# Kernel tuning notes

Measured on AMD Instinct MI355X. Metric: run time of the kernel, lower is better.

The kernel has to match this reference:

```python
import jax, jax.numpy as jnp
import numpy as np

B, Z, H, T = 256, 512, 1024, 512   # batch, z_size, hidden (conductor==decoder), num_tokens
L, N = 16, 16                      # num_levels, notes_per_bar


def setup_inputs() -> dict:
    key = jax.random.key(0)
    ks = jax.random.split(key, 16)
    s = 0.05  # weight init scale
    rn = lambda k, shp, sc=1.0: sc * jax.random.normal(k, shp, dtype=jnp.float32)
    return {
        "z": rn(ks[0], (B, L * N, 1, Z)),
        "dec_h0": rn(ks[1], (L, B, H)),
        "dec_c0": rn(ks[2], (L, B, H)),
        # linear_in (computed but unused by the original forward)
        "lin_in_W": rn(ks[3], (Z, Z), s), "lin_in_b": rn(ks[4], (Z,), s),
        # conductor LSTM (input Z -> hidden H), PyTorch gate order i,f,g,o
        "cond_Wih": rn(ks[5], (4 * H, Z), s), "cond_Whh": rn(ks[6], (4 * H, H), s),
        "cond_bih": rn(ks[7], (4 * H,), s), "cond_bhh": rn(ks[8], (4 * H,), s),
        # decoder LSTM (input T+H -> hidden H)
        "dec_Wih": rn(ks[9], (4 * H, T + H), s), "dec_Whh": rn(ks[10], (4 * H, H), s),
        "dec_bih": rn(ks[11], (4 * H,), s), "dec_bhh": rn(ks[12], (4 * H,), s),
        # output projection
        "out_W": rn(ks[13], (T, H), s), "out_b": rn(ks[14], (T,), s),
    }


def _lstm_cell(x, h, c, Wih, Whh, b):
    gates = x @ Wih.T + h @ Whh.T + b            # [B, 4H]
    i, f, g, o = jnp.split(gates, 4, axis=-1)
    c = jax.nn.sigmoid(f) * c + jax.nn.sigmoid(i) * jnp.tanh(g)
    h = jax.nn.sigmoid(o) * jnp.tanh(c)
    return h, c


def reference(z, dec_h0, dec_c0, lin_in_W, lin_in_b,
              cond_Wih, cond_Whh, cond_bih, cond_bhh,
              dec_Wih, dec_Whh, dec_bih, dec_bhh, out_W, out_b):
    Bsz = z.shape[0]
    Tt = out_b.shape[0]
    Hh = cond_Whh.shape[1]

    _unused = z @ lin_in_W.T + lin_in_b  # linear_in output is discarded in the source

    cond_b = cond_bih + cond_bhh
    dec_b = dec_bih + dec_bhh

    # conductor consumes z[:, L*level, 0, :] for each level
    z_lv = jnp.transpose(z[:, jnp.arange(L) * L, 0, :], (1, 0, 2))  # [L, B, Z]

    def level_step(carry, xs):
        ch, cc = carry
        zl, dh, dc = xs
        ch, cc = _lstm_cell(zl, ch, cc, cond_Wih, cond_Whh, cond_b)
        emb = ch  # [B, H], fixed conductor embedding for this bar

        def note_step(c2, _):
            note, dh2, dc2 = c2
            inp = jnp.concatenate([emb, note], axis=-1)  # [B, H+T]
            dh2, dc2 = _lstm_cell(inp, dh2, dc2, dec_Wih, dec_Whh, dec_b)
            out = jax.nn.sigmoid(dh2 @ out_W.T + out_b)  # [B, T]
            return (out, dh2, dc2), out

        note0 = jnp.zeros((Bsz, Tt), dtype=z.dtype)
        _, outs = jax.lax.scan(note_step, (note0, dh, dc), None, length=N)  # [N, B, T]
        return (ch, cc), outs

    h0 = jnp.zeros((Bsz, Hh), dtype=z.dtype)
    _, all_outs = jax.lax.scan(level_step, (h0, h0), (z_lv, dec_h0, dec_c0))  # [L, N, B, T]
    notes = jnp.transpose(all_outs, (2, 0, 1, 3)).reshape(Bsz, L * N, Tt)
    return notes
```

## Files before the change

### kernel.cpp

```cpp
#include <hip/hip_runtime.h>

typedef __bf16 bf16;
typedef __attribute__((ext_vector_type(8))) __bf16 bf16x8;
typedef __attribute__((ext_vector_type(4))) float f32x4;

__device__ __forceinline__ void gload_lds16(const void* g, void* l) {
  __builtin_amdgcn_global_load_lds(
      (const __attribute__((address_space(1))) void*)g,
      (__attribute__((address_space(3))) void*)l, 16, 0, 0);
}

__device__ __forceinline__ float sigmoidf_(float x) { return 1.0f / (1.0f + expf(-x)); }

template<int BM, int BN, int WM, int WN, int MODE>
__global__ __launch_bounds__(WM * WN * 64)
void gemm_bt(const bf16* __restrict__ A, int lda,
             const bf16* __restrict__ Bw, int ldb,
             float* __restrict__ C, int ldc,
             int K,
             const float* __restrict__ outb, float* __restrict__ dout,
             bf16* __restrict__ anote, int nstep) {
  constexpr int BK = 64;
  constexpr int THREADS = WM * WN * 64;
  constexpr int SM = BM / WM, SN = BN / WN;
  constexpr int FM = SM / 16, FN = SN / 16;

  __shared__ __align__(16) bf16 lsA[BM * BK];
  __shared__ __align__(16) bf16 lsB[BN * BK];

  const int tid = threadIdx.x;
  const int lane = tid & 63;
  const int wave = tid >> 6;
  const int wm = wave / WN, wn = wave % WN;
  const int m0 = blockIdx.y * BM;
  const int n0 = blockIdx.x * BN;

  f32x4 acc[FM][FN] = {};

  const bf16* gA = A + (size_t)m0 * lda;
  const bf16* gB = Bw + (size_t)n0 * ldb;

  for (int k0 = 0; k0 < K; k0 += BK) {
#pragma unroll
    for (int i = 0; i < (BM * 8) / THREADS; ++i) {
      int idx = i * THREADS + tid;
      gload_lds16(gA + (size_t)(idx >> 3) * lda + k0 + (idx & 7) * 8, &lsA[idx * 8]);
    }
#pragma unroll
    for (int i = 0; i < (BN * 8) / THREADS; ++i) {
      int idx = i * THREADS + tid;
      gload_lds16(gB + (size_t)(idx >> 3) * ldb + k0 + (idx & 7) * 8, &lsB[idx * 8]);
    }
    __syncthreads();

#pragma unroll
    for (int kk = 0; kk < BK; kk += 32) {
      bf16x8 av[FM], bv[FN];
#pragma unroll
      for (int i = 0; i < FM; ++i)
        av[i] = *(const bf16x8*)&lsA[(wm * SM + i * 16 + (lane & 15)) * BK + kk + (lane >> 4) * 8];
#pragma unroll
      for (int j = 0; j < FN; ++j)
        bv[j] = *(const bf16x8*)&lsB[(wn * SN + j * 16 + (lane & 15)) * BK + kk + (lane >> 4) * 8];
#pragma unroll
      for (int i = 0; i < FM; ++i)
#pragma unroll
        for (int j = 0; j < FN; ++j)
          acc[i][j] = __builtin_amdgcn_mfma_f32_16x16x32_bf16(av[i], bv[j], acc[i][j], 0, 0, 0);
    }
    __syncthreads();
  }

#pragma unroll
  for (int i = 0; i < FM; ++i) {
#pragma unroll
    for (int j = 0; j < FN; ++j) {
      const int col = n0 + wn * SN + j * 16 + (lane & 15);
      const int rbase = m0 + wm * SM + i * 16 + ((lane >> 4) << 2);
#pragma unroll
      for (int r = 0; r < 4; ++r) {
        const int row = rbase + r;
        float v = acc[i][j][r];
        if constexpr (MODE == 0) {
          C[(size_t)row * ldc + col] = v;
        } else if constexpr (MODE == 2) {
          ((bf16*)C)[(size_t)row * ldc + col] = (bf16)v;
        } else {
          v = sigmoidf_(v + outb[col]);
          const int l = row >> 8, b = row & 255;
          dout[((size_t)(b * 256 + l * 16 + nstep)) * 512 + col] = v;
          anote[(size_t)row * 1536 + col] = (bf16)v;
        }
      }
    }
  }
}

template<int BM, int BJ, int WM, int WJ>
__global__ __launch_bounds__(WM * WJ * 64, 2)
void gemm_cell(const bf16* __restrict__ A, int lda,
               const bf16* __restrict__ Bw,
               const bf16* __restrict__ X,
               const float* __restrict__ bias,
               float* __restrict__ cst,
               bf16* __restrict__ hout, int ldh, int K) {
  constexpr int BK = 64;
  constexpr int THREADS = WM * WJ * 64;
  constexpr int BN = BJ * 64;
  constexpr int SM = BM / WM;
  constexpr int TJ = BJ / WJ;
  constexpr int FM = SM / 16;

  __shared__ __align__(16) bf16 lsA[BM * BK];
  __shared__ __align__(16) bf16 lsB[BN * BK];

  const int tid = threadIdx.x;
  const int lane = tid & 63;
  const int wave = tid >> 6;
  const int wm = wave / WJ, wj = wave % WJ;
  const int m0 = blockIdx.y * BM;
  const int qb = blockIdx.x * BJ;

  f32x4 acc[FM][TJ][4] = {};

  const bf16* gA = A + (size_t)m0 * lda;
  const bf16* gB = Bw + (size_t)(qb * 64) * K;

  for (int k0 = 0; k0 < K; k0 += BK) {
#pragma unroll
    for (int i = 0; i < (BM * 8) / THREADS; ++i) {
      int idx = i * THREADS + tid;
      gload_lds16(gA + (size_t)(idx >> 3) * lda + k0 + (idx & 7) * 8, &lsA[idx * 8]);
    }
#pragma unroll
    for (int i = 0; i < (BN * 8) / THREADS; ++i) {
      int idx = i * THREADS + tid;
      gload_lds16(gB + (size_t)(idx >> 3) * K + k0 + (idx & 7) * 8, &lsB[idx * 8]);
    }
    __syncthreads();

#pragma unroll
    for (int kk = 0; kk < BK; kk += 32) {
      bf16x8 av[FM], bv[TJ][4];
#pragma unroll
      for (int i = 0; i < FM; ++i)
        av[i] = *(const bf16x8*)&lsA[(wm * SM + i * 16 + (lane & 15)) * BK + kk + (lane >> 4) * 8];
#pragma unroll
      for (int t = 0; t < TJ; ++t)
#pragma unroll
        for (int g = 0; g < 4; ++g)
          bv[t][g] = *(const bf16x8*)
              &lsB[((wj * TJ + t) * 64 + g * 16 + (lane & 15)) * BK + kk + (lane >> 4) * 8];
#pragma unroll
      for (int i = 0; i < FM; ++i)
#pragma unroll
        for (int t = 0; t < TJ; ++t)
#pragma unroll
          for (int g = 0; g < 4; ++g)
            acc[i][t][g] =
                __builtin_amdgcn_mfma_f32_16x16x32_bf16(av[i], bv[t][g], acc[i][t][g], 0, 0, 0);
    }
    __syncthreads();
  }

#pragma unroll
  for (int i = 0; i < FM; ++i) {
#pragma unroll
    for (int t = 0; t < TJ; ++t) {
      const int q = qb + wj * TJ + t;
      const int jj = lane & 15;
      const int j = q * 16 + jj;
      const int rbase = m0 + wm * SM + i * 16 + ((lane >> 4) << 2);
      const float b0 = bias[q * 64 + jj];
      const float b1 = bias[q * 64 + 16 + jj];
      const float b2 = bias[q * 64 + 32 + jj];
      const float b3 = bias[q * 64 + 48 + jj];
#pragma unroll
      for (int r = 0; r < 4; ++r) {
        const int row = rbase + r;
        const bf16* xp = X + (size_t)row * 4096 + q * 64 + jj;
        const float gi = acc[i][t][0][r] + (float)xp[0]  + b0;
        const float gf = acc[i][t][1][r] + (float)xp[16] + b1;
        const float gg = acc[i][t][2][r] + (float)xp[32] + b2;
        const float go = acc[i][t][3][r] + (float)xp[48] + b3;
        const size_t ci = (size_t)row * 1024 + j;
        const float c = sigmoidf_(gf) * cst[ci] + sigmoidf_(gi) * tanhf(gg);
        cst[ci] = c;
        hout[(size_t)row * ldh + j] = (bf16)(sigmoidf_(go) * tanhf(c));
      }
    }
  }
}


__global__ void conv_f32_bf16(const float* __restrict__ src, bf16* __restrict__ dst, int n) {
  int idx = blockIdx.x * 256 + threadIdx.x;
  if (idx < n) dst[idx] = (bf16)src[idx];
}

__device__ __forceinline__ int p_src_row(int n) {
  int q = n >> 6, gate = (n >> 4) & 3, jj = n & 15;
  return gate * 1024 + q * 16 + jj;
}

__global__ void pack_w_dec(const float* __restrict__ wih, const float* __restrict__ whh,
                           bf16* __restrict__ dst) {
  int idx = blockIdx.x * 256 + threadIdx.x;
  int n = idx / 1536, c = idx - n * 1536;
  int r = p_src_row(n);
  float v = (c < 512) ? wih[(size_t)r * 1536 + 1024 + c] : whh[(size_t)r * 1024 + (c - 512)];
  dst[idx] = (bf16)v;
}

__global__ void pack_w_emb(const float* __restrict__ wih, bf16* __restrict__ dst) {
  int idx = blockIdx.x * 256 + threadIdx.x;
  int n = idx >> 10, c = idx & 1023;
  dst[idx] = (bf16)wih[(size_t)p_src_row(n) * 1536 + c];
}

__global__ void pack_w_perm(const float* __restrict__ src, bf16* __restrict__ dst, int Kw) {
  int idx = blockIdx.x * 256 + threadIdx.x;
  int n = idx / Kw, c = idx - n * Kw;
  dst[idx] = (bf16)src[(size_t)p_src_row(n) * Kw + c];
}

__global__ void pack_bias(const float* __restrict__ bih, const float* __restrict__ bhh,
                          float* __restrict__ dst) {
  int n = blockIdx.x * 256 + threadIdx.x;
  int r = p_src_row(n);
  dst[n] = bih[r] + bhh[r];
}

__global__ void pack_zb(const float* __restrict__ z, bf16* __restrict__ dst) {
  int idx = blockIdx.x * 256 + threadIdx.x;
  int m = idx >> 9, k = idx & 511;
  int l = m >> 8, b = m & 255;
  dst[idx] = (bf16)z[((size_t)b * 256 + 16 * l) * 512 + k];
}

__global__ void init_cond(float* __restrict__ cc, bf16* __restrict__ hz0) {
  int idx = blockIdx.x * 256 + threadIdx.x;
  cc[idx] = 0.f;
  hz0[idx] = (bf16)0.f;
}

__global__ void init_state(const float* __restrict__ h0, const float* __restrict__ c0,
                           bf16* __restrict__ Abuf, float* __restrict__ cdec) {
  int idx = blockIdx.x * 256 + threadIdx.x;
  int m = idx / 1536, c = idx - m * 1536;
  if (c < 512) {
    Abuf[idx] = (bf16)0.f;
  } else {
    int j = c - 512;
    size_t s = (size_t)m * 1024 + j;
    Abuf[idx] = (bf16)h0[s];
    cdec[s] = c0[s];
  }
}

extern "C" void kernel_launch(void* const* d_in, const int* in_sizes, int n_in,
                              void* d_out, int out_size, void* d_ws, size_t ws_size,
                              hipStream_t stream) {
  const float* z        = (const float*)d_in[0];
  const float* dec_h0   = (const float*)d_in[1];
  const float* dec_c0   = (const float*)d_in[2];
  const float* cond_Wih = (const float*)d_in[5];
  const float* cond_Whh = (const float*)d_in[6];
  const float* cond_bih = (const float*)d_in[7];
  const float* cond_bhh = (const float*)d_in[8];
  const float* dec_Wih  = (const float*)d_in[9];
  const float* dec_Whh  = (const float*)d_in[10];
  const float* dec_bih  = (const float*)d_in[11];
  const float* dec_bhh  = (const float*)d_in[12];
  const float* out_W    = (const float*)d_in[13];
  const float* out_b    = (const float*)d_in[14];
  float* out = (float*)d_out;

  char* ws = (char*)d_ws;
  size_t off = 0;
  auto alloc = [&](size_t bytes) {
    void* p = ws + off;
    off += (bytes + 255) & ~(size_t)255;
    return p;
  };
  bf16* E    = (bf16*)alloc(4096ull * 4096 * 2);
  bf16* Xz   = (bf16*)alloc(4096ull * 4096 * 2);
  float* cdec = (float*)alloc(4096ull * 1024 * 4);
  bf16* Abuf  = (bf16*)alloc(4096ull * 1536 * 2);
  bf16* Wd    = (bf16*)alloc(4096ull * 1536 * 2);
  bf16* We    = (bf16*)alloc(4096ull * 1024 * 2);
  bf16* Wcih  = (bf16*)alloc(4096ull * 512 * 2);
  bf16* Wchh  = (bf16*)alloc(4096ull * 1024 * 2);
  bf16* Wo    = (bf16*)alloc(512ull * 1024 * 2);
  float* cc   = (float*)alloc(256ull * 1024 * 4);
  bf16* emb   = (bf16*)alloc(4096ull * 1024 * 2);
  bf16* Zb    = (bf16*)alloc(4096ull * 512 * 2);
  bf16* hz0   = (bf16*)alloc(256ull * 1024 * 2);
  float* bdP  = (float*)alloc(4096ull * 4);
  float* bcP  = (float*)alloc(4096ull * 4);

  dim3 b256(256);

  pack_w_perm<<<4096 * 512 / 256, b256, 0, stream>>>(cond_Wih, Wcih, 512);
  pack_w_perm<<<4096 * 1024 / 256, b256, 0, stream>>>(cond_Whh, Wchh, 1024);
  conv_f32_bf16<<<(512 * 1024 + 255) / 256, b256, 0, stream>>>(out_W, Wo, 512 * 1024);
  pack_w_dec<<<4096 * 1536 / 256, b256, 0, stream>>>(dec_Wih, dec_Whh, Wd);
  pack_w_emb<<<4096 * 1024 / 256, b256, 0, stream>>>(dec_Wih, We);
  pack_bias<<<16, b256, 0, stream>>>(dec_bih, dec_bhh, bdP);
  pack_bias<<<16, b256, 0, stream>>>(cond_bih, cond_bhh, bcP);
  pack_zb<<<4096 * 512 / 256, b256, 0, stream>>>(z, Zb);
  init_cond<<<256 * 1024 / 256, b256, 0, stream>>>(cc, hz0);
  init_state<<<4096 * 1536 / 256, b256, 0, stream>>>(dec_h0, dec_c0, Abuf, cdec);

  gemm_bt<128, 128, 2, 2, 2><<<dim3(32, 32), dim3(256), 0, stream>>>(
      Zb, 512, Wcih, 512, (float*)Xz, 4096, 512, nullptr, nullptr, nullptr, 0);

  for (int l = 0; l < 16; ++l) {
    const bf16* hprev = (l == 0) ? hz0 : (emb + (size_t)(l - 1) * 256 * 1024);
    gemm_cell<32, 2, 2, 2><<<dim3(32, 8), dim3(256), 0, stream>>>(
        hprev, 1024, Wchh, Xz + (size_t)l * 256 * 4096, bcP,
        cc, emb + (size_t)l * 256 * 1024, 1024, 1024);
  }

  gemm_bt<128, 128, 2, 2, 2><<<dim3(32, 32), dim3(256), 0, stream>>>(
      emb, 1024, We, 1024, (float*)E, 4096, 1024, nullptr, nullptr, nullptr, 0);

  for (int n = 0; n < 16; ++n) {
    gemm_cell<128, 4, 2, 2><<<dim3(16, 32), dim3(256), 0, stream>>>(
        Abuf, 1536, Wd, E, bdP, cdec, Abuf + 512, 1536, 1536);
    gemm_bt<128, 64, 2, 2, 1><<<dim3(512 / 64, 4096 / 128), dim3(256), 0, stream>>>(
        Abuf + 512, 1536, Wo, 1024, nullptr, 0, 1024, out_b, out, Abuf, n);
  }
}
```

Before: 1.979 ms.

## Add 256x256 double-buffered 8-wave GEMM kernel for large GEMMs and decoder cell

Introduces a new gemm8 kernel with 256x256 tiles, 512 threads, swizzled LDS via global_load_lds, double buffering with two-ahead prefetch, sched barriers and setprio to interleave loads with MFMA. It replaces the two precompute GEMMs (Xz, E) and the per-note decoder LSTM cell GEMM with fused gate epilogue. The aim is higher MFMA utilisation and fewer LDS/global stalls on the dominant 4096x4096x1536 recurrent GEMM. The trade-off is only 256 workgroups, with 128KB LDS each, which may limit occupancy and tail balance.

```diff
diff --git a/kernel.cpp b/kernel.cpp
--- a/kernel.cpp
+++ b/kernel.cpp
@@ -12,12 +12,191 @@
 
 __device__ __forceinline__ float sigmoidf_(float x) { return 1.0f / (1.0f + expf(-x)); }
 
+#define SB() __builtin_amdgcn_sched_barrier(0)
+#define BAR()                          \
+  do {                                 \
+    SB();                              \
+    __builtin_amdgcn_s_barrier();      \
+    SB();                              \
+  } while (0)
+
+template<int MODE>
+__global__ __launch_bounds__(512, 2)
+void gemm8(const bf16* __restrict__ A, int lda,
+           const bf16* __restrict__ Bw, int K,
+           bf16* __restrict__ Cb,
+           const bf16* __restrict__ X, const float* __restrict__ bias,
+           float* __restrict__ cst, bf16* __restrict__ hout, int ldh) {
+  extern __shared__ __align__(16) char smem_raw[];
+  bf16* lsA = (bf16*)smem_raw;
+  bf16* lsB = lsA + 2 * 16384;
+
+  const int tid = threadIdx.x;
+  const int lane = tid & 63;
+  const int wave = tid >> 6;
+  const int wm = wave >> 2, wn = wave & 3;
+
+  const int bid = blockIdx.x;
+  const int wgid = (bid & 7) * 32 + (bid >> 3);
+  const int m0 = (wgid >> 4) * 256, n0 = (wgid & 15) * 256;
+
+  const int nkt = K >> 6;
+
+  const int srow = tid >> 3;
+  const int csw = ((tid & 7) * 8) ^ (((tid >> 5) & 1) << 4);
+  const bf16* gA = A + (size_t)m0 * lda + csw;
+  const bf16* gB = Bw + (size_t)n0 * K + csw;
+
+  auto stageA = [&](int c, int h, int kt) {
+    bf16* d = lsA + c * 16384 + h * 8192 + tid * 8;
+    const bf16* s = gA + (size_t)(h * 128 + srow) * lda + kt * 64;
+    gload_lds16(s, d);
+    gload_lds16(s + (size_t)64 * lda, d + 4096);
+  };
+  auto stageB = [&](int c, int h, int kt) {
+    bf16* d = lsB + c * 16384 + h * 8192 + tid * 8;
+    const bf16* s = gB + (size_t)(h * 128 + srow) * K + kt * 64;
+    gload_lds16(s, d);
+    gload_lds16(s + (size_t)64 * K, d + 4096);
+  };
+
+  const int sw16 = ((lane >> 2) & 1) << 4;
+  const int c0 = (((lane >> 4) * 8)) ^ sw16;
+  const int c1 = (32 + ((lane >> 4) * 8)) ^ sw16;
+  const int arow = (wm * 128 + (lane & 15)) * 64;
+  const int brow = (wn * 64 + (lane & 15)) * 64;
+
+  f32x4 acc[8][4] = {};
+
+  stageA(0, 0, 0); stageA(0, 1, 0); stageB(0, 0, 0); stageB(0, 1, 0);
+  if (nkt > 1) { stageA(1, 0, 1); stageA(1, 1, 1); stageB(1, 0, 1); stageB(1, 1, 1); }
+  if (nkt > 1) asm volatile("s_waitcnt vmcnt(8)" ::: "memory");
+  else         asm volatile("s_waitcnt vmcnt(0)" ::: "memory");
+  BAR();
+
+  for (int t = 0; t < nkt; ++t) {
+    const int c = t & 1;
+    const bf16* pA = lsA + c * 16384;
+    const bf16* pB = lsB + c * 16384;
+    const bool pre = (t + 2 < nkt);
+
+    bf16x8 av[4][2], bv[4][2];
+
+#pragma unroll
+    for (int f = 0; f < 4; ++f) {
+      av[f][0] = *(const bf16x8*)&pA[arow + f * 1024 + c0];
+      av[f][1] = *(const bf16x8*)&pA[arow + f * 1024 + c1];
+    }
+#pragma unroll
+    for (int g = 0; g < 2; ++g) {
+      bv[g][0] = *(const bf16x8*)&pB[brow + g * 1024 + c0];
+      bv[g][1] = *(const bf16x8*)&pB[brow + g * 1024 + c1];
+    }
+    BAR();
+    __builtin_amdgcn_s_setprio(1);
+#pragma unroll
+    for (int f = 0; f < 4; ++f)
+#pragma unroll
+      for (int g = 0; g < 2; ++g) {
+        acc[f][g] = __builtin_amdgcn_mfma_f32_16x16x32_bf16(av[f][0], bv[g][0], acc[f][g], 0, 0, 0);
+        acc[f][g] = __builtin_amdgcn_mfma_f32_16x16x32_bf16(av[f][1], bv[g][1], acc[f][g], 0, 0, 0);
+      }
+    __builtin_amdgcn_s_setprio(0);
+    BAR();
+
+#pragma unroll
+    for (int g = 2; g < 4; ++g) {
+      bv[g][0] = *(const bf16x8*)&pB[brow + g * 1024 + c0];
+      bv[g][1] = *(const bf16x8*)&pB[brow + g * 1024 + c1];
+    }
+    BAR();
+    __builtin_amdgcn_s_setprio(1);
+#pragma unroll
+    for (int f = 0; f < 4; ++f)
+#pragma unroll
+      for (int g = 2; g < 4; ++g) {
+        acc[f][g] = __builtin_amdgcn_mfma_f32_16x16x32_bf16(av[f][0], bv[g][0], acc[f][g], 0, 0, 0);
+        acc[f][g] = __builtin_amdgcn_mfma_f32_16x16x32_bf16(av[f][1], bv[g][1], acc[f][g], 0, 0, 0);
+      }
+    __builtin_amdgcn_s_setprio(0);
+    BAR();
+
+    if (pre) { stageB(c, 0, t + 2); stageB(c, 1, t + 2); }
+#pragma unroll
+    for (int f = 0; f < 4; ++f) {
+      av[f][0] = *(const bf16x8*)&pA[arow + (f + 4) * 1024 + c0];
+      av[f][1] = *(const bf16x8*)&pA[arow + (f + 4) * 1024 + c1];
+    }
+    BAR();
+    __builtin_amdgcn_s_setprio(1);
+#pragma unroll
+    for (int f = 0; f < 4; ++f)
+#pragma unroll
+      for (int g = 0; g < 2; ++g) {
+        acc[f + 4][g] = __builtin_amdgcn_mfma_f32_16x16x32_bf16(av[f][0], bv[g][0], acc[f + 4][g], 0, 0, 0);
+        acc[f + 4][g] = __builtin_amdgcn_mfma_f32_16x16x32_bf16(av[f][1], bv[g][1], acc[f + 4][g], 0, 0, 0);
+      }
+    __builtin_amdgcn_s_setprio(0);
+    BAR();
+
+    if (pre) { stageA(c, 0, t + 2); stageA(c, 1, t + 2); }
+    SB();
+    __builtin_amdgcn_s_setprio(1);
+#pragma unroll
+    for (int f = 0; f < 4; ++f)
+#pragma unroll
+      for (int g = 2; g < 4; ++g) {
+        acc[f + 4][g] = __builtin_amdgcn_mfma_f32_16x16x32_bf16(av[f][0], bv[g][0], acc[f + 4][g], 0, 0, 0);
+        acc[f + 4][g] = __builtin_amdgcn_mfma_f32_16x16x32_bf16(av[f][1], bv[g][1], acc[f + 4][g], 0, 0, 0);
+      }
+    __builtin_amdgcn_s_setprio(0);
+    if (pre) asm volatile("s_waitcnt vmcnt(8)" ::: "memory");
+    else     asm volatile("s_waitcnt vmcnt(0)" ::: "memory");
+    BAR();
+  }
+
+  const int jj = lane & 15;
+  const int rb = m0 + wm * 128 + ((lane >> 4) << 2);
+  if constexpr (MODE == 0) {
+    const int col0 = n0 + wn * 64 + jj;
+#pragma unroll
+    for (int f = 0; f < 8; ++f)
+#pragma unroll
+      for (int g = 0; g < 4; ++g)
+#pragma unroll
+        for (int r = 0; r < 4; ++r)
+          Cb[(size_t)(rb + f * 16 + r) * 4096 + col0 + g * 16] = (bf16)acc[f][g][r];
+  } else {
+    const int q = (n0 >> 6) + wn;
+    const int j = q * 16 + jj;
+    const float b0 = bias[q * 64 + jj];
+    const float b1 = bias[q * 64 + 16 + jj];
+    const float b2 = bias[q * 64 + 32 + jj];
+    const float b3 = bias[q * 64 + 48 + jj];
+#pragma unroll
+    for (int f = 0; f < 8; ++f) {
+#pragma unroll
+      for (int r = 0; r < 4; ++r) {
+        const int row = rb + f * 16 + r;
+        const bf16* xp = X + (size_t)row * 4096 + q * 64 + jj;
+        const float gi = acc[f][0][r] + (float)xp[0] + b0;
+        const float gf = acc[f][1][r] + (float)xp[16] + b1;
+        const float gg = acc[f][2][r] + (float)xp[32] + b2;
+        const float go = acc[f][3][r] + (float)xp[48] + b3;
+        const size_t ci = (size_t)row * 1024 + j;
+        const float cn = sigmoidf_(gf) * cst[ci] + sigmoidf_(gi) * tanhf(gg);
+        cst[ci] = cn;
+        hout[(size_t)row * ldh + j] = (bf16)(sigmoidf_(go) * tanhf(cn));
+      }
+    }
+  }
+}
+
 template<int BM, int BN, int WM, int WN, int MODE>
 __global__ __launch_bounds__(WM * WN * 64)
 void gemm_bt(const bf16* __restrict__ A, int lda,
              const bf16* __restrict__ Bw, int ldb,
-             float* __restrict__ C, int ldc,
-             int K,
+             float* __restrict__ C, int ldc, int K,
              const float* __restrict__ outb, float* __restrict__ dout,
              bf16* __restrict__ anote, int nstep) {
   constexpr int BK = 64;
@@ -83,8 +262,6 @@
         float v = acc[i][j][r];
         if constexpr (MODE == 0) {
           C[(size_t)row * ldc + col] = v;
-        } else if constexpr (MODE == 2) {
-          ((bf16*)C)[(size_t)row * ldc + col] = (bf16)v;
         } else {
           v = sigmoidf_(v + outb[col]);
           const int l = row >> 8, b = row & 255;
@@ -179,7 +356,7 @@
       for (int r = 0; r < 4; ++r) {
         const int row = rbase + r;
         const bf16* xp = X + (size_t)row * 4096 + q * 64 + jj;
-        const float gi = acc[i][t][0][r] + (float)xp[0]  + b0;
+        const float gi = acc[i][t][0][r] + (float)xp[0] + b0;
         const float gf = acc[i][t][1][r] + (float)xp[16] + b1;
         const float gg = acc[i][t][2][r] + (float)xp[32] + b2;
         const float go = acc[i][t][3][r] + (float)xp[48] + b3;
@@ -283,8 +460,8 @@
     off += (bytes + 255) & ~(size_t)255;
     return p;
   };
-  bf16* E    = (bf16*)alloc(4096ull * 4096 * 2);
-  bf16* Xz   = (bf16*)alloc(4096ull * 4096 * 2);
+  bf16* E     = (bf16*)alloc(4096ull * 4096 * 2);
+  bf16* Xz    = (bf16*)alloc(4096ull * 4096 * 2);
   float* cdec = (float*)alloc(4096ull * 1024 * 4);
   bf16* Abuf  = (bf16*)alloc(4096ull * 1536 * 2);
   bf16* Wd    = (bf16*)alloc(4096ull * 1536 * 2);
@@ -301,6 +478,11 @@
 
   dim3 b256(256);
 
+  hipFuncSetAttribute(reinterpret_cast<const void*>(&gemm8<0>),
+                      hipFuncAttributeMaxDynamicSharedMemorySize, 131072);
+  hipFuncSetAttribute(reinterpret_cast<const void*>(&gemm8<1>),
+                      hipFuncAttributeMaxDynamicSharedMemorySize, 131072);
+
   pack_w_perm<<<4096 * 512 / 256, b256, 0, stream>>>(cond_Wih, Wcih, 512);
   pack_w_perm<<<4096 * 1024 / 256, b256, 0, stream>>>(cond_Whh, Wchh, 1024);
   conv_f32_bf16<<<(512 * 1024 + 255) / 256, b256, 0, stream>>>(out_W, Wo, 512 * 1024);
@@ -312,8 +494,8 @@
   init_cond<<<256 * 1024 / 256, b256, 0, stream>>>(cc, hz0);
   init_state<<<4096 * 1536 / 256, b256, 0, stream>>>(dec_h0, dec_c0, Abuf, cdec);
 
-  gemm_bt<128, 128, 2, 2, 2><<<dim3(32, 32), dim3(256), 0, stream>>>(
-      Zb, 512, Wcih, 512, (float*)Xz, 4096, 512, nullptr, nullptr, nullptr, 0);
+  gemm8<0><<<256, 512, 131072, stream>>>(Zb, 512, Wcih, 512, Xz,
+                                         nullptr, nullptr, nullptr, nullptr, 0);
 
   for (int l = 0; l < 16; ++l) {
     const bf16* hprev = (l == 0) ? hz0 : (emb + (size_t)(l - 1) * 256 * 1024);
@@ -322,12 +504,12 @@
         cc, emb + (size_t)l * 256 * 1024, 1024, 1024);
   }
 
-  gemm_bt<128, 128, 2, 2, 2><<<dim3(32, 32), dim3(256), 0, stream>>>(
-      emb, 1024, We, 1024, (float*)E, 4096, 1024, nullptr, nullptr, nullptr, 0);
+  gemm8<0><<<256, 512, 131072, stream>>>(emb, 1024, We, 1024, E,
+                                         nullptr, nullptr, nullptr, nullptr, 0);
 
   for (int n = 0; n < 16; ++n) {
-    gemm_cell<128, 4, 2, 2><<<dim3(16, 32), dim3(256), 0, stream>>>(
-        Abuf, 1536, Wd, E, bdP, cdec, Abuf + 512, 1536, 1536);
+    gemm8<1><<<256, 512, 131072, stream>>>(Abuf, 1536, Wd, 1536, nullptr,
+                                           E, bdP, cdec, Abuf + 512, 1536);
     gemm_bt<128, 64, 2, 2, 1><<<dim3(512 / 64, 4096 / 128), dim3(256), 0, stream>>>(
         Abuf + 512, 1536, Wo, 1024, nullptr, 0, 1024, out_b, out, Abuf, n);
   }
```

After: 1.880 ms. 5.0% less time.
